# Performance work log

Hardware: AMD Instinct MI355X
Metric: run time of the kernel (lower is better)

Reference implementation:

```python
import jax, jax.numpy as jnp
import numpy as np

N, E, F_IN, H, G, C = 130000, 260000, 300, 128, 128, 2

def _lin_init(key, out_f, in_f):
    kw, kb = jax.random.split(key)
    s = 1.0 / np.sqrt(in_f).astype(np.float32)
    W = jax.random.uniform(kw, (out_f, in_f), jnp.float32, -s, s)
    b = jax.random.uniform(kb, (out_f,), jnp.float32, -s, s)
    return W, b

def setup_inputs():
    key = jax.random.key(0)
    ks = jax.random.split(key, 8)
    x = jax.random.normal(ks[0], (N, F_IN), jnp.float32)
    edge_index = jax.random.randint(ks[1], (2, E), 0, N)
    batch = jnp.sort(jax.random.randint(ks[2], (N,), 0, G))
    # SAGEConv: lin_l (neighbors, with bias) and lin_r (root, no bias)
    Wl, bl = _lin_init(ks[3], H, F_IN)
    Wr, _ = _lin_init(ks[4], H, F_IN)
    W0, b0 = _lin_init(ks[5], H, F_IN)          # lin0
    W1, b1 = _lin_init(ks[6], H, 2 * H)          # lin1
    W2, b2 = _lin_init(ks[7], C, H)              # lin2
    return {"x": x, "edge_index": edge_index, "batch": batch,
            "Wl": Wl, "bl": bl, "Wr": Wr,
            "W0": W0, "b0": b0, "W1": W1, "b1": b1, "W2": W2, "b2": b2}

def reference(x, edge_index, batch, Wl, bl, Wr, W0, b0, W1, b1, W2, b2):
    src, dst = edge_index[0], edge_index[1]
    # SAGEConv (mean aggregation): messages flow src -> dst
    msg_sum = jax.ops.segment_sum(x[src], dst, num_segments=N)          # [N, F_IN]
    deg = jax.ops.segment_sum(jnp.ones((E,), x.dtype), dst, num_segments=N)
    agg = msg_sum / jnp.maximum(deg, 1.0)[:, None]
    h = jax.nn.relu(agg @ Wl.T + bl + x @ Wr.T)                          # [N, H]
    # global_max_pool over sorted batch vector
    h = jax.ops.segment_max(h, batch, num_segments=G)                    # [G, H]
    # root node = first node of each graph (batch is sorted, all graphs present)
    root = jnp.searchsorted(batch, jnp.arange(G), side='left')           # [G]
    news = jax.nn.relu(x[root] @ W0.T + b0)                              # [G, H]
    h = jax.nn.relu(jnp.concatenate([news, h], axis=-1) @ W1.T + b1)     # [G, H]
    h = h @ W2.T + b2                                                    # [G, C]
    return jax.nn.log_softmax(h, axis=-1)
```

## Files before the change

kernel.cpp:

```cpp
#include <hip/hip_runtime.h>
#include <hip/hip_bf16.h>
#include <math.h>

#define F_IN 300
#define HDIM 128
#define HO   256
#define KP   320
#define NKS  10
#define CLS  2
#define MB   64
#define NPB  64
#define CHUNK 1024
#define PROJ_BLOCKS 512

typedef short short8 __attribute__((ext_vector_type(8)));
typedef float f32x4 __attribute__((ext_vector_type(4)));

static __device__ __forceinline__ unsigned short f2bf(float f) {
    union { float f; unsigned int u; } v; v.f = f;
    unsigned int u = v.u;
    unsigned int r = (u + 0x7FFFu + ((u >> 16) & 1u)) >> 16;
    return (unsigned short)r;
}
static __device__ __forceinline__ float bf2f(unsigned short h) {
    union { unsigned int u; float f; } v; v.u = ((unsigned int)h) << 16;
    return v.f;
}

__global__ __launch_bounds__(256) void prepw_kernel(const float* __restrict__ Wl,
                                                    const float* __restrict__ Wr,
                                                    unsigned short* __restrict__ Wb) {
    int i = blockIdx.x * 256 + threadIdx.x;
    if (i >= KP * HO) return;
    int j   = i & 7;
    int c15 = (i >> 3) & 15;
    int hi  = (i >> 7) & 3;
    int ctk = i >> 9;
    int ct  = ctk & 15;
    int ks  = ctk >> 4;
    int k = ks * 32 + hi * 8 + j;
    int c = ct * 16 + c15;
    float v = 0.f;
    if (k < F_IN) v = (c < HDIM) ? Wl[c * F_IN + k] : Wr[(c - HDIM) * F_IN + k];
    Wb[i] = f2bf(v);
}

__global__ __launch_bounds__(512, 4) void proj_kernel(const float* __restrict__ x,
                                                      const unsigned short* __restrict__ Wb,
                                                      unsigned short* __restrict__ xPb,
                                                      int N, int ntiles) {
    __shared__ unsigned short xs[MB * KP];
    int tid = threadIdx.x;
    int lane = tid & 63, w = tid >> 6;
    int lo = lane & 15, hi = lane >> 4;

    short8 bfrag[NKS][2];
#pragma unroll
    for (int ks = 0; ks < NKS; ++ks)
#pragma unroll
        for (int c = 0; c < 2; ++c) {
            int ct = 2 * w + c;
            bfrag[ks][c] = *reinterpret_cast<const short8*>(
                Wb + (size_t)(ks * 16 + ct) * 512 + hi * 128 + lo * 8);
        }

    char* xsb = (char*)xs;

    for (int tile = blockIdx.x; tile < ntiles; tile += gridDim.x) {
        int n0 = tile * MB;

#pragma unroll
        for (int it = 0; it < 5; ++it) {
            int idx = tid + it * 512;
            int row = idx / 40;
            int g   = idx - row * 40;
            int k0  = g * 8;
            int gr  = n0 + row;
            float vf[8];
#pragma unroll
            for (int j = 0; j < 8; ++j) vf[j] = 0.f;
            if (gr < N) {
                const float* xr = x + (size_t)gr * F_IN;
                if (k0 + 8 <= F_IN) {
                    float4 v0 = *reinterpret_cast<const float4*>(xr + k0);
                    float4 v1 = *reinterpret_cast<const float4*>(xr + k0 + 4);
                    vf[0]=v0.x; vf[1]=v0.y; vf[2]=v0.z; vf[3]=v0.w;
                    vf[4]=v1.x; vf[5]=v1.y; vf[6]=v1.z; vf[7]=v1.w;
                } else if (k0 < F_IN) {
#pragma unroll
                    for (int j = 0; j < 8; ++j) if (k0 + j < F_IN) vf[j] = xr[k0 + j];
                }
            }
            unsigned short tmp[8];
#pragma unroll
            for (int j = 0; j < 8; ++j) tmp[j] = f2bf(vf[j]);
            int boff = g * 1024 + ((row ^ (g & 7)) << 4);
            *reinterpret_cast<short8*>(xsb + boff) = *reinterpret_cast<const short8*>(tmp);
        }
        __syncthreads();

        f32x4 acc[4][2];
#pragma unroll
        for (int r = 0; r < 4; ++r) {
            acc[r][0] = (f32x4){0.f, 0.f, 0.f, 0.f};
            acc[r][1] = (f32x4){0.f, 0.f, 0.f, 0.f};
        }
#pragma unroll
        for (int ks = 0; ks < NKS; ++ks) {
            int g = ks * 4 + hi;
            int lob = g * 1024 + ((lo ^ (g & 7)) << 4);
#pragma unroll
            for (int r = 0; r < 4; ++r) {
                short8 a = *reinterpret_cast<const short8*>(xsb + lob + r * 256);
                acc[r][0] = __builtin_amdgcn_mfma_f32_16x16x32_bf16(a, bfrag[ks][0], acc[r][0], 0, 0, 0);
                acc[r][1] = __builtin_amdgcn_mfma_f32_16x16x32_bf16(a, bfrag[ks][1], acc[r][1], 0, 0, 0);
            }
        }

#pragma unroll
        for (int r = 0; r < 4; ++r)
#pragma unroll
            for (int c = 0; c < 2; ++c)
#pragma unroll
                for (int rr = 0; rr < 4; ++rr) {
                    int row = n0 + r * 16 + hi * 4 + rr;
                    if (row < N)
                        xPb[(size_t)row * HO + (2 * w + c) * 16 + lo] = f2bf(acc[r][c][rr]);
                }
        __syncthreads();
    }
}

__global__ __launch_bounds__(256) void count_kernel(const int* __restrict__ ei,
                                                    int* __restrict__ cnt, int E) {
    int e = blockIdx.x * 256 + threadIdx.x;
    if (e >= E) return;
    atomicAdd(&cnt[ei[E + e]], 1);
}

__global__ __launch_bounds__(256) void scan1_kernel(const int* __restrict__ cnt,
                                                    int* __restrict__ tmp,
                                                    int* __restrict__ bsum, int N) {
    __shared__ int ssum[256];
    int t = threadIdx.x;
    int base = blockIdx.x * CHUNK + t * 4;
    int c[4];
#pragma unroll
    for (int j = 0; j < 4; ++j) c[j] = (base + j < N) ? cnt[base + j] : 0;
    int s = c[0] + c[1] + c[2] + c[3];
    ssum[t] = s;
    __syncthreads();
    for (int off = 1; off < 256; off <<= 1) {
        int a = (t >= off) ? ssum[t - off] : 0;
        __syncthreads();
        ssum[t] += a;
        __syncthreads();
    }
    int run = ssum[t] - s;
#pragma unroll
    for (int j = 0; j < 4; ++j) {
        if (base + j < N) tmp[base + j] = run;
        run += c[j];
    }
    if (t == 255) bsum[blockIdx.x] = ssum[255];
}

__global__ __launch_bounds__(256) void scan2_kernel(int* __restrict__ bsum, int nb) {
    __shared__ int sd[256];
    int t = threadIdx.x;
    int v = (t < nb) ? bsum[t] : 0;
    sd[t] = v;
    __syncthreads();
    for (int off = 1; off < 256; off <<= 1) {
        int a = (t >= off) ? sd[t - off] : 0;
        __syncthreads();
        sd[t] += a;
        __syncthreads();
    }
    if (t < nb) bsum[t] = sd[t] - v;
}

__global__ __launch_bounds__(256) void scan3_kernel(const int* __restrict__ tmp,
                                                    const int* __restrict__ bsum,
                                                    int* __restrict__ rowptr,
                                                    int* __restrict__ cursor, int N) {
    int i = blockIdx.x * 256 + threadIdx.x;
    if (i >= N) return;
    int v = tmp[i] + bsum[i >> 10];
    rowptr[i] = v;
    cursor[i] = v;
}

__global__ __launch_bounds__(256) void fill_kernel(const int* __restrict__ ei,
                                                   int* __restrict__ cursor,
                                                   int* __restrict__ srcl, int E) {
    int e = blockIdx.x * 256 + threadIdx.x;
    if (e >= E) return;
    int s = ei[e];
    int d = ei[E + e];
    int pos = atomicAdd(&cursor[d], 1);
    srcl[pos] = s;
}

__global__ __launch_bounds__(128) void gather_pool_kernel(const unsigned short* __restrict__ xPb,
                                                          const int* __restrict__ rowptr,
                                                          const int* __restrict__ rowend,
                                                          const int* __restrict__ srcl,
                                                          const float* __restrict__ bl,
                                                          const int* __restrict__ batch,
                                                          float* __restrict__ gpool, int N) {
    int t = threadIdx.x;
    int n0 = blockIdx.x * NPB;
    if (n0 >= N) return;
    float blv = bl[t];
    float runmax = 0.f;
    int curg = batch[n0];
    int nmax = N - n0; if (nmax > NPB) nmax = NPB;
    for (int i = 0; i < nmax; ++i) {
        int n = n0 + i;
        int gb = batch[n];
        if (gb != curg) {
            atomicMax((unsigned int*)&gpool[curg * HDIM + t], __float_as_uint(runmax));
            runmax = 0.f;
            curg = gb;
        }
        int e0 = rowptr[n];
        int e1 = rowend[n];
        float acc = 0.f;
        for (int e = e0; e < e1; ++e) {
            int s = srcl[e];
            acc += bf2f(xPb[(size_t)s * HO + t]);
        }
        float rv = 1.0f / fmaxf((float)(e1 - e0), 1.0f);
        float h = fmaf(acc, rv, blv + bf2f(xPb[(size_t)n * HO + HDIM + t]));
        h = fmaxf(h, 0.f);
        runmax = fmaxf(runmax, h);
    }
    atomicMax((unsigned int*)&gpool[curg * HDIM + t], __float_as_uint(runmax));
}

__global__ __launch_bounds__(256) void root_kernel(const int* __restrict__ batch,
                                                   int* __restrict__ root, int N) {
    int i = blockIdx.x * 256 + threadIdx.x;
    if (i >= N) return;
    if (i == 0 || batch[i] != batch[i - 1]) root[batch[i]] = i;
}

__global__ __launch_bounds__(128) void final_kernel(const float* __restrict__ x,
                                                    const int* __restrict__ root,
                                                    const float* __restrict__ gpool,
                                                    const float* __restrict__ W0,
                                                    const float* __restrict__ b0,
                                                    const float* __restrict__ W1,
                                                    const float* __restrict__ b1,
                                                    const float* __restrict__ W2,
                                                    const float* __restrict__ b2,
                                                    float* __restrict__ out) {
    __shared__ float xrow[F_IN];
    __shared__ float cat[HO];
    __shared__ float h1s[HDIM];
    __shared__ float part[2][2];
    int g = blockIdx.x, t = threadIdx.x;
    int r = root[g];
    const float* xr = x + (size_t)r * F_IN;
    for (int k = t; k < F_IN; k += HDIM) xrow[k] = xr[k];
    __syncthreads();

    float a = b0[t];
    const float* w0r = W0 + t * F_IN;
    for (int k = 0; k < F_IN; ++k) a = fmaf(xrow[k], w0r[k], a);
    cat[t] = fmaxf(a, 0.f);
    cat[HDIM + t] = gpool[g * HDIM + t];
    __syncthreads();

    float s = b1[t];
    const float* w1r = W1 + t * HO;
    for (int k = 0; k < HO; ++k) s = fmaf(cat[k], w1r[k], s);
    h1s[t] = fmaxf(s, 0.f);
    __syncthreads();

    float hv = h1s[t];
    float p0 = hv * W2[t];
    float p1 = hv * W2[HDIM + t];
#pragma unroll
    for (int o2 = 32; o2 > 0; o2 >>= 1) {
        p0 += __shfl_down(p0, o2);
        p1 += __shfl_down(p1, o2);
    }
    int lane = t & 63, wv = t >> 6;
    if (lane == 0) { part[0][wv] = p0; part[1][wv] = p1; }
    __syncthreads();
    if (t == 0) {
        float z0 = part[0][0] + part[0][1] + b2[0];
        float z1 = part[1][0] + part[1][1] + b2[1];
        float m = fmaxf(z0, z1);
        float lse = m + logf(expf(z0 - m) + expf(z1 - m));
        out[g * CLS + 0] = z0 - lse;
        out[g * CLS + 1] = z1 - lse;
    }
}

extern "C" void kernel_launch(void* const* d_in, const int* in_sizes, int n_in,
                              void* d_out, int out_size, void* d_ws, size_t ws_size,
                              hipStream_t stream) {
    const float* x     = (const float*)d_in[0];
    const int*   ei    = (const int*)d_in[1];
    const int*   batch = (const int*)d_in[2];
    const float* Wl    = (const float*)d_in[3];
    const float* bl    = (const float*)d_in[4];
    const float* Wr    = (const float*)d_in[5];
    const float* W0    = (const float*)d_in[6];
    const float* b0    = (const float*)d_in[7];
    const float* W1    = (const float*)d_in[8];
    const float* b1    = (const float*)d_in[9];
    const float* W2    = (const float*)d_in[10];
    const float* b2    = (const float*)d_in[11];
    float* out = (float*)d_out;

    int N = in_sizes[2];
    int E = in_sizes[1] / 2;
    int G = out_size / CLS;

    char* ws = (char*)d_ws;
    size_t off = 0;
    auto carve = [&](size_t bytes) -> void* {
        void* p = ws + off;
        off += (bytes + 255) & ~(size_t)255;
        return p;
    };
    unsigned short* xPb = (unsigned short*)carve((size_t)N * HO * sizeof(unsigned short));
    char*  zbeg   = ws + off;
    int*   cnt    = (int*)carve((size_t)N * sizeof(int));
    float* gpool  = (float*)carve((size_t)G * HDIM * sizeof(float));
    char*  zend   = ws + off;
    int*   tmp    = (int*)carve((size_t)N * sizeof(int));
    int*   rowptr = (int*)carve((size_t)N * sizeof(int));
    int*   cursor = (int*)carve((size_t)N * sizeof(int));
    int*   srcl   = (int*)carve((size_t)E * sizeof(int));
    int*   bsum   = (int*)carve(1024 * sizeof(int));
    unsigned short* Wb = (unsigned short*)carve((size_t)KP * HO * sizeof(unsigned short));
    int*   root   = (int*)carve((size_t)G * sizeof(int));
    (void)ws_size; (void)n_in;

    int nb = (N + CHUNK - 1) / CHUNK;
    int ntiles = (N + MB - 1) / MB;
    int pblocks = ntiles < PROJ_BLOCKS ? ntiles : PROJ_BLOCKS;

    hipMemsetAsync(zbeg, 0, (size_t)(zend - zbeg), stream);

    prepw_kernel<<<(KP * HO + 255) / 256, 256, 0, stream>>>(Wl, Wr, Wb);
    proj_kernel<<<pblocks, 512, 0, stream>>>(x, Wb, xPb, N, ntiles);

    count_kernel<<<(E + 255) / 256, 256, 0, stream>>>(ei, cnt, E);
    scan1_kernel<<<nb, 256, 0, stream>>>(cnt, tmp, bsum, N);
    scan2_kernel<<<1, 256, 0, stream>>>(bsum, nb);
    scan3_kernel<<<(N + 255) / 256, 256, 0, stream>>>(tmp, bsum, rowptr, cursor, N);
    fill_kernel<<<(E + 255) / 256, 256, 0, stream>>>(ei, cursor, srcl, E);

    gather_pool_kernel<<<(N + NPB - 1) / NPB, HDIM, 0, stream>>>(xPb, rowptr, cursor, srcl,
                                                                 bl, batch, gpool, N);
    root_kernel<<<(N + 255) / 256, 256, 0, stream>>>(batch, root, N);
    final_kernel<<<G, HDIM, 0, stream>>>(x, root, gpool, W0, b0, W1, b1, W2, b2, out);
}
```

Before: 212.6 us.

## Double-buffer projection tiles with register prefetch and vectorized transposed output stores

The projection kernel now prefetches the next tile of x into registers while computing MFMAs on the current tile held in one of two shared-memory buffers. It then writes the next tile into the other buffer, so only one barrier per tile is needed. The MFMA operands are swapped so each lane holds four consecutive output columns, which allows packed 8-byte bf16 stores in place of scalar 2-byte stores. This doubles LDS use, drops the occupancy hint and raises register pressure from the prefetch registers, which may lower occupancy.

After: 254.6 us. 19.8% more time.

```diff
diff --git a/kernel.cpp b/kernel.cpp
--- a/kernel.cpp
+++ b/kernel.cpp
@@ -45,60 +45,82 @@
     Wb[i] = f2bf(v);
 }
 
-__global__ __launch_bounds__(512, 4) void proj_kernel(const float* __restrict__ x,
-                                                      const unsigned short* __restrict__ Wb,
-                                                      unsigned short* __restrict__ xPb,
-                                                      int N, int ntiles) {
-    __shared__ unsigned short xs[MB * KP];
+__global__ __launch_bounds__(512) void proj_kernel(const float* __restrict__ x,
+                                                   const unsigned short* __restrict__ Wb,
+                                                   unsigned short* __restrict__ xPb,
+                                                   int N, int ntiles) {
+    __shared__ unsigned short xs[2][MB * KP];
     int tid = threadIdx.x;
     int lane = tid & 63, w = tid >> 6;
     int lo = lane & 15, hi = lane >> 4;
 
-    short8 bfrag[NKS][2];
+    short8 wfrag[NKS][2];
 #pragma unroll
     for (int ks = 0; ks < NKS; ++ks)
 #pragma unroll
         for (int c = 0; c < 2; ++c) {
             int ct = 2 * w + c;
-            bfrag[ks][c] = *reinterpret_cast<const short8*>(
+            wfrag[ks][c] = *reinterpret_cast<const short8*>(
                 Wb + (size_t)(ks * 16 + ct) * 512 + hi * 128 + lo * 8);
         }
 
-    char* xsb = (char*)xs;
-
-    for (int tile = blockIdx.x; tile < ntiles; tile += gridDim.x) {
+    int srow[5], sg[5];
+#pragma unroll
+    for (int it = 0; it < 5; ++it) {
+        int idx = tid + it * 512;
+        srow[it] = idx / 40;
+        sg[it]   = idx - srow[it] * 40;
+    }
+
+    float4 pre[5][2];
+
+    auto stage_load = [&](int tile) {
         int n0 = tile * MB;
-
 #pragma unroll
         for (int it = 0; it < 5; ++it) {
-            int idx = tid + it * 512;
-            int row = idx / 40;
-            int g   = idx - row * 40;
-            int k0  = g * 8;
-            int gr  = n0 + row;
-            float vf[8];
-#pragma unroll
-            for (int j = 0; j < 8; ++j) vf[j] = 0.f;
+            int k0 = sg[it] * 8;
+            int gr = n0 + srow[it];
+            float4 z = {0.f, 0.f, 0.f, 0.f};
+            pre[it][0] = z; pre[it][1] = z;
             if (gr < N) {
                 const float* xr = x + (size_t)gr * F_IN;
                 if (k0 + 8 <= F_IN) {
-                    float4 v0 = *reinterpret_cast<const float4*>(xr + k0);
-                    float4 v1 = *reinterpret_cast<const float4*>(xr + k0 + 4);
-                    vf[0]=v0.x; vf[1]=v0.y; vf[2]=v0.z; vf[3]=v0.w;
-                    vf[4]=v1.x; vf[5]=v1.y; vf[6]=v1.z; vf[7]=v1.w;
+                    pre[it][0] = *reinterpret_cast<const float4*>(xr + k0);
+                    pre[it][1] = *reinterpret_cast<const float4*>(xr + k0 + 4);
                 } else if (k0 < F_IN) {
-#pragma unroll
-                    for (int j = 0; j < 8; ++j) if (k0 + j < F_IN) vf[j] = xr[k0 + j];
+                    pre[it][0] = *reinterpret_cast<const float4*>(xr + k0);
                 }
             }
+        }
+    };
+
+    auto stage_write = [&](char* xsb) {
+#pragma unroll
+        for (int it = 0; it < 5; ++it) {
+            int g = sg[it], row = srow[it];
             unsigned short tmp[8];
-#pragma unroll
-            for (int j = 0; j < 8; ++j) tmp[j] = f2bf(vf[j]);
+            tmp[0] = f2bf(pre[it][0].x); tmp[1] = f2bf(pre[it][0].y);
+            tmp[2] = f2bf(pre[it][0].z); tmp[3] = f2bf(pre[it][0].w);
+            tmp[4] = f2bf(pre[it][1].x); tmp[5] = f2bf(pre[it][1].y);
+            tmp[6] = f2bf(pre[it][1].z); tmp[7] = f2bf(pre[it][1].w);
             int boff = g * 1024 + ((row ^ (g & 7)) << 4);
             *reinterpret_cast<short8*>(xsb + boff) = *reinterpret_cast<const short8*>(tmp);
         }
-        __syncthreads();
-
+    };
+
+    int tile = blockIdx.x;
+    if (tile >= ntiles) return;
+
+    stage_load(tile);
+    stage_write((char*)xs[0]);
+    __syncthreads();
+
+    int p = 0;
+    while (tile < ntiles) {
+        int nxt = tile + gridDim.x;
+        if (nxt < ntiles) stage_load(nxt);
+
+        char* xsb = (char*)xs[p];
         f32x4 acc[4][2];
 #pragma unroll
         for (int r = 0; r < 4; ++r) {
@@ -112,22 +134,31 @@
 #pragma unroll
             for (int r = 0; r < 4; ++r) {
                 short8 a = *reinterpret_cast<const short8*>(xsb + lob + r * 256);
-                acc[r][0] = __builtin_amdgcn_mfma_f32_16x16x32_bf16(a, bfrag[ks][0], acc[r][0], 0, 0, 0);
-                acc[r][1] = __builtin_amdgcn_mfma_f32_16x16x32_bf16(a, bfrag[ks][1], acc[r][1], 0, 0, 0);
+                acc[r][0] = __builtin_amdgcn_mfma_f32_16x16x32_bf16(wfrag[ks][0], a, acc[r][0], 0, 0, 0);
+                acc[r][1] = __builtin_amdgcn_mfma_f32_16x16x32_bf16(wfrag[ks][1], a, acc[r][1], 0, 0, 0);
             }
         }
 
-#pragma unroll
-        for (int r = 0; r < 4; ++r)
-#pragma unroll
-            for (int c = 0; c < 2; ++c)
-#pragma unroll
-                for (int rr = 0; rr < 4; ++rr) {
-                    int row = n0 + r * 16 + hi * 4 + rr;
-                    if (row < N)
-                        xPb[(size_t)row * HO + (2 * w + c) * 16 + lo] = f2bf(acc[r][c][rr]);
+        int n0 = tile * MB;
+#pragma unroll
+        for (int r = 0; r < 4; ++r) {
+            int row = n0 + r * 16 + lo;
+            if (row < N) {
+#pragma unroll
+                for (int c = 0; c < 2; ++c) {
+                    unsigned short pk[4];
+                    pk[0] = f2bf(acc[r][c][0]); pk[1] = f2bf(acc[r][c][1]);
+                    pk[2] = f2bf(acc[r][c][2]); pk[3] = f2bf(acc[r][c][3]);
+                    *reinterpret_cast<uint2*>(xPb + (size_t)row * HO + (2 * w + c) * 16 + hi * 4) =
+                        *reinterpret_cast<const uint2*>(pk);
                 }
-        __syncthreads();
+            }
+        }
+
+        if (nxt < ntiles) stage_write((char*)xs[p ^ 1]);
+        __syncthreads();
+        p ^= 1;
+        tile = nxt;
     }
 }
 
```
